# Performance work log

Measured on AMD Instinct MI355X. Metric: run time of the kernel, lower is better.

Reference implementation:

```python
import jax, jax.numpy as jnp
from jax import lax
import numpy as np

B, T = 16, 256
E, H, V = 512, 1024, 32000

def setup_inputs() -> dict:
    key = jax.random.key(0)
    ks = jax.random.split(key, 10)
    s = lambda fan_in: 1.0 / np.sqrt(fan_in)
    return {
        "z": jax.random.normal(ks[0], (B, H), dtype=jnp.float32),
        "x": jax.random.randint(ks[1], (B, T), 0, V, dtype=jnp.int64),
        "emb_table": jax.random.normal(ks[2], (V, E), dtype=jnp.float32) * 0.02,
        "W_init": jax.random.uniform(ks[3], (H, H), jnp.float32, -s(H), s(H)),
        "b_init": jnp.zeros((H,), jnp.float32),
        "W_ih": jax.random.uniform(ks[4], (3 * H, E), jnp.float32, -s(H), s(H)),
        "W_hh": jax.random.uniform(ks[5], (3 * H, H), jnp.float32, -s(H), s(H)),
        "b_ih": jax.random.uniform(ks[6], (3 * H,), jnp.float32, -s(H), s(H)),
        "b_hh": jax.random.uniform(ks[7], (3 * H,), jnp.float32, -s(H), s(H)),
        "W_out": jax.random.uniform(ks[8], (V, H), jnp.float32, -s(H), s(H)),
        "b_out": jnp.zeros((V,), jnp.float32),
    }

def reference(z, x, emb_table, W_init, b_init, W_ih, W_hh, b_ih, b_hh, W_out, b_out):
    # h0 = tanh(aff_init_lm(z))
    h0 = jnp.tanh(z @ W_init.T + b_init)  # [B, H]
    xe = emb_table[x]                      # [B, T, E] embedding lookup
    # Precompute input-side gate projections for all timesteps (no recurrence on input side)
    gi_all = jnp.einsum('bte,ge->btg', xe, W_ih) + b_ih  # [B, T, 3H]

    def step(h, gi):
        gh = h @ W_hh.T + b_hh                 # [B, 3H]
        ir, iz, inn = jnp.split(gi, 3, axis=-1)
        hr, hz, hn = jnp.split(gh, 3, axis=-1)
        r = jax.nn.sigmoid(ir + hr)
        zg = jax.nn.sigmoid(iz + hz)
        n = jnp.tanh(inn + r * hn)
        h_new = (1.0 - zg) * n + zg * h
        # Original module emits aff_out_x(h[j]) (state BEFORE consuming token j),
        # so we output the PREVIOUS hidden state at each step.
        return h_new, h

    _, hs_prev = lax.scan(step, h0, jnp.swapaxes(gi_all, 0, 1))  # [T, B, H] = h0..h_{T-1}
    hs = jnp.swapaxes(hs_prev, 0, 1)                              # [B, T, H]
    logits = jnp.einsum('bth,vh->btv', hs, W_out) + b_out         # [B, T, V]
    return logits
```

## Files before the change

kernel.cpp:

```cpp
#include <hip/hip_runtime.h>

typedef __attribute__((ext_vector_type(8))) short bf16x8;
typedef __attribute__((ext_vector_type(8))) unsigned short ushort8;
typedef __attribute__((ext_vector_type(4))) float f32x4;
typedef __attribute__((ext_vector_type(4))) int i32x4;

__device__ __forceinline__ unsigned short f2bf(float f) {
  union { float f; unsigned u; } v; v.f = f;
  unsigned r = (v.u + 0x7FFFu + ((v.u >> 16) & 1u)) >> 16;
  return (unsigned short)r;
}
__device__ __forceinline__ float bf2f(unsigned short h) {
  union { unsigned u; float f; } v; v.u = ((unsigned)h) << 16;
  return v.f;
}
__device__ __forceinline__ float sigm(float x) { return 1.f / (1.f + __expf(-x)); }
__device__ __forceinline__ float tanh_(float x) { return 1.f - 2.f / (__expf(2.f * x) + 1.f); }

__device__ __forceinline__ i32x4 ld_coh_b128(const void* p) {
  i32x4 r;
  asm volatile("global_load_dwordx4 %0, %1, off sc0 sc1" : "=v"(r) : "v"(p) : "memory");
  return r;
}
__device__ __forceinline__ unsigned ld_coh_u16(const void* p) {
  unsigned r;
  asm volatile("global_load_ushort %0, %1, off sc0 sc1" : "=v"(r) : "v"(p) : "memory");
  return r;
}
__device__ __forceinline__ void st_coh_b128(void* p, i32x4 v) {
  asm volatile("global_store_dwordx4 %0, %1, off sc0 sc1" :: "v"(p), "v"(v) : "memory");
}
__device__ __forceinline__ void st_coh_b16(void* p, unsigned v) {
  asm volatile("global_store_short %0, %1, off sc0 sc1" :: "v"(p), "v"(v) : "memory");
}
__device__ __forceinline__ void wait_vm0_fence() {
  asm volatile("s_waitcnt vmcnt(0)" ::: "memory");
  __builtin_amdgcn_sched_barrier(0);
}

#define GLDS(g, l) __builtin_amdgcn_global_load_lds( \
    (const __attribute__((address_space(1))) unsigned int*)(g), \
    (__attribute__((address_space(3))) unsigned int*)(l), 16, 0, 0)

__global__ __launch_bounds__(256) void prep(
    const int* __restrict__ x, const float* __restrict__ emb, unsigned short* __restrict__ xe,
    const float* __restrict__ z, const float* __restrict__ Wi, const float* __restrict__ bi,
    float* __restrict__ h0f, unsigned short* __restrict__ hb16,
    const float* __restrict__ Wih, unsigned short* __restrict__ WihB,
    const float* __restrict__ Wout, unsigned short* __restrict__ WoutB) {
  const int tid = threadIdx.x;
  const unsigned bid = blockIdx.x;
  if (bid < 2048) {
    const int r = (bid << 1) + (tid >> 7);
    const int b = r & 15, t = r >> 4;
    const int tok = x[b * 256 + t];
    const int c = tid & 127;
    const float4 v = ((const float4*)(emb + (size_t)tok * 512))[c];
    ushort4 o; o.x = f2bf(v.x); o.y = f2bf(v.y); o.z = f2bf(v.z); o.w = f2bf(v.w);
    ((ushort4*)(xe + (size_t)r * 512))[c] = o;
  } else if (bid < 2112) {
    const int idx = (bid - 2048) * 256 + tid;
    const int b = idx & 15, i = idx >> 4;
    const float4* wr = (const float4*)(Wi + (size_t)i * 1024);
    const float4* zr = (const float4*)(z + (size_t)b * 1024);
    float acc = bi[i];
#pragma unroll 4
    for (int k = 0; k < 256; ++k) {
      float4 w = wr[k], zv = zr[k];
      acc += w.x * zv.x + w.y * zv.y + w.z * zv.z + w.w * zv.w;
    }
    const float h = tanh_(acc);
    h0f[(size_t)b * 1024 + i] = h;
    hb16[((i >> 4) << 8) + (b << 4) + (i & 15)] = f2bf(h);
  } else if (bid < 3648) {
    const int i = (int)(bid - 2112) * 256 + tid;
    const float4 v = ((const float4*)Wih)[i];
    ushort4 o; o.x = f2bf(v.x); o.y = f2bf(v.y); o.z = f2bf(v.z); o.w = f2bf(v.w);
    ((ushort4*)WihB)[i] = o;
  } else {
    for (int i = (int)(bid - 3648) * 256 + tid; i < 32000 * 1024 / 4; i += 512 * 256) {
      const float4 v = ((const float4*)Wout)[i];
      ushort4 o; o.x = f2bf(v.x); o.y = f2bf(v.y); o.z = f2bf(v.z); o.w = f2bf(v.w);
      ((ushort4*)WoutB)[i] = o;
    }
  }
}

__global__ __launch_bounds__(512, 1) void mega(
    const float* __restrict__ Whh, const float* __restrict__ bhh,
    unsigned short* __restrict__ gi, const float* __restrict__ h0f,
    unsigned short* __restrict__ hb16, unsigned short* __restrict__ hs,
    unsigned int* __restrict__ flags, unsigned int* __restrict__ gicnt,
    const unsigned short* __restrict__ xe, const unsigned short* __restrict__ WihB,
    const float* __restrict__ bih,
    const unsigned short* __restrict__ WoutB, const float* __restrict__ bout,
    float* __restrict__ out) {
  __shared__ __align__(16) char lds[65536];
  const int tid = threadIdx.x, lane = tid & 63, wave = tid >> 6;

  if (blockIdx.x < 64) {
    const int j = blockIdx.x;
    if (tid >= 256) {
      for (int t = 0; t < 256; ++t) { __syncthreads(); if (t < 255) __syncthreads(); }
      __syncthreads();
      return;
    }
    float (*ghp)[16][48] = (float (*)[16][48])lds;
    unsigned short (*hsl)[16] = (unsigned short (*)[16])(lds + 12288);

    const int lr = lane & 15;
    const int hi8 = (lane >> 4) << 3;
    const int kw = wave << 8;

    bf16x8 wf[3][8];
#pragma unroll
    for (int n = 0; n < 3; ++n) {
      const float* wrow = Whh + (size_t)(n * 1024 + (j << 4) + lr) * 1024 + kw + hi8;
#pragma unroll
      for (int ki = 0; ki < 8; ++ki) {
        const float4 u = *(const float4*)(wrow + ki * 32);
        const float4 v = *(const float4*)(wrow + ki * 32 + 4);
        bf16x8 w;
        w[0] = (short)f2bf(u.x); w[1] = (short)f2bf(u.y);
        w[2] = (short)f2bf(u.z); w[3] = (short)f2bf(u.w);
        w[4] = (short)f2bf(v.x); w[5] = (short)f2bf(v.y);
        w[6] = (short)f2bf(v.z); w[7] = (short)f2bf(v.w);
        wf[n][ki] = w;
      }
    }

    const int b = tid >> 4, c = tid & 15;
    const int cg = (j << 4) + c;
    float hreg = h0f[(size_t)b * 1024 + cg];
    const float br = bhh[cg], bz = bhh[1024 + cg], bn = bhh[2048 + cg];

    for (int t = 0; t < 256; ++t) {
      {
        long guard = 0;
        for (;;) {
          bool ok = true;
          if (t > 0) {
            const unsigned f = __hip_atomic_load(&flags[lane << 5], __ATOMIC_RELAXED,
                                                 __HIP_MEMORY_SCOPE_AGENT);
            ok = (f >= (unsigned)t);
          }
          const unsigned g2 = __hip_atomic_load(&gicnt[(t >> 3) << 5], __ATOMIC_RELAXED,
                                                __HIP_MEMORY_SCOPE_AGENT);
          ok = ok && (g2 >= 24u);
          if (__all(ok)) break;
          __builtin_amdgcn_s_sleep(1);
          if (++guard > (1L << 20)) break;
        }
      }

      const unsigned short* base = hb16 + ((t & 1) << 14);
      i32x4 hv[8];
#pragma unroll
      for (int ki = 0; ki < 8; ++ki) {
        const int kk = kw + (ki << 5) + hi8;
        hv[ki] = ld_coh_b128(base + ((kk >> 4) << 8) + (lr << 4) + (kk & 15));
      }
      const char* gbase = (const char*)gi + ((size_t)((t << 4) + b) * 3072 + cg) * 2;
      const unsigned uir = ld_coh_u16(gbase);
      const unsigned uiz = ld_coh_u16(gbase + 2048);
      const unsigned uin = ld_coh_u16(gbase + 4096);
      wait_vm0_fence();

      f32x4 acc[3] = {};
#pragma unroll
      for (int ki = 0; ki < 8; ++ki) {
        const bf16x8 af = __builtin_bit_cast(bf16x8, hv[ki]);
#pragma unroll
        for (int n = 0; n < 3; ++n)
          acc[n] = __builtin_amdgcn_mfma_f32_16x16x32_bf16(af, wf[n][ki], acc[n], 0, 0, 0);
      }
#pragma unroll
      for (int n = 0; n < 3; ++n)
#pragma unroll
        for (int q = 0; q < 4; ++q)
          ghp[wave][(lane >> 4) * 4 + q][n * 16 + lr] = acc[n][q];
      __syncthreads();

      const float ir = bf2f((unsigned short)uir);
      const float iz = bf2f((unsigned short)uiz);
      const float inn = bf2f((unsigned short)uin);
      const float hr = ghp[0][b][c]      + ghp[1][b][c]      + ghp[2][b][c]      + ghp[3][b][c];
      const float hz = ghp[0][b][16 + c] + ghp[1][b][16 + c] + ghp[2][b][16 + c] + ghp[3][b][16 + c];
      const float hn = ghp[0][b][32 + c] + ghp[1][b][32 + c] + ghp[2][b][32 + c] + ghp[3][b][32 + c];
      const float rg = sigm(ir + hr + br);
      const float zg = sigm(iz + hz + bz);
      const float ng = tanh_(inn + rg * (hn + bn));
      const float hprev = hreg;
      hreg = (1.f - zg) * ng + zg * hprev;

      if (t < 255) {
        hsl[b][c] = f2bf(hreg);
        __syncthreads();
        unsigned short* nb = hb16 + (((t + 1) & 1) << 14) + (j << 8);
        if (tid < 32) {
          const i32x4 v = *(const i32x4*)&hsl[tid >> 1][(tid & 1) << 3];
          st_coh_b128(nb + (tid << 3), v);
        }
        if (wave == 0)
          asm volatile("s_waitcnt vmcnt(0)" ::: "memory");
        if (tid == 0)
          __hip_atomic_store(&flags[j << 5], (unsigned)(t + 1),
                             __ATOMIC_RELAXED, __HIP_MEMORY_SCOPE_AGENT);
      }

      st_coh_b16(hs + ((size_t)((t << 4) + b) << 10) + cg, (unsigned)f2bf(hprev));
    }
    asm volatile("s_waitcnt vmcnt(0)" ::: "memory");
    __syncthreads();
    if (tid == 0)
      __hip_atomic_store(&flags[j << 5], 1024u, __ATOMIC_RELAXED, __HIP_MEMORY_SCOPE_AGENT);
    return;
  }

  if (blockIdx.x < 832) {
    const int g = blockIdx.x - 64;
    const int tm = g / 24, tn = g % 24;
    const long row0 = (long)tm << 7, col0 = (long)tn << 7;
    char* As = lds;
    char* Bs = lds + 8192;
    char* Ct = lds + 16384;

    const int sr = tid >> 2, sk = (tid & 3) << 3;
    const unsigned short* Abase = xe + (row0 + sr) * 512 + sk;
    const unsigned short* Bbase = WihB + (col0 + sr) * 512 + sk;
    char* ldsA = As + wave * 1024;
    char* ldsB = Bs + wave * 1024;

    const int wm2 = (wave >> 2) << 6, wn2 = (wave & 3) << 5;
    const int lr = lane & 15, lk = (lane >> 4) << 3;
    f32x4 acc[4][2] = {};

    for (int k0 = 0; k0 < 512; k0 += 32) {
      __syncthreads();
      GLDS(Abase + k0, ldsA);
      GLDS(Bbase + k0, ldsB);
      __syncthreads();
      bf16x8 af[4], bfr[2];
#pragma unroll
      for (int i = 0; i < 4; ++i)
        af[i] = *(const bf16x8*)(As + ((wm2 + i * 16 + lr) * 32 + lk) * 2);
#pragma unroll
      for (int jj = 0; jj < 2; ++jj)
        bfr[jj] = *(const bf16x8*)(Bs + ((wn2 + jj * 16 + lr) * 32 + lk) * 2);
#pragma unroll
      for (int i = 0; i < 4; ++i)
#pragma unroll
        for (int jj = 0; jj < 2; ++jj)
          acc[i][jj] = __builtin_amdgcn_mfma_f32_16x16x32_bf16(af[i], bfr[jj], acc[i][jj], 0, 0, 0);
    }

    const int lq = (lane >> 4) << 2;
    float bias0 = bih[col0 + wn2 + lr], bias1 = bih[col0 + wn2 + 16 + lr];
    __syncthreads();
#pragma unroll
    for (int i = 0; i < 4; ++i)
#pragma unroll
      for (int jj = 0; jj < 2; ++jj)
#pragma unroll
        for (int q = 0; q < 4; ++q)
          *(unsigned short*)(Ct + (wm2 + i * 16 + lq + q) * 256
                                + ((wn2 + jj * 16 + lr) << 1)) =
              f2bf(acc[i][jj][q] + (jj ? bias1 : bias0));
    __syncthreads();
#pragma unroll
    for (int k2 = 0; k2 < 4; ++k2) {
      const int s2 = (k2 << 9) + tid;
      const int row = s2 >> 4, colb = (s2 & 15) << 4;
      st_coh_b128((char*)gi + (size_t)(row0 + row) * 6144 + (col0 << 1) + colb,
                  *(const i32x4*)(Ct + row * 256 + colb));
    }
    asm volatile("s_waitcnt vmcnt(0)" ::: "memory");
    __syncthreads();
    if (tid == 0)
      __hip_atomic_fetch_add(&gicnt[tm << 5], 1u, __ATOMIC_RELAXED,
                             __HIP_MEMORY_SCOPE_AGENT);
    return;
  }

  const int gb = blockIdx.x - 832;
  const int bm = gb / 125, bn = gb % 125;
  const long row0 = (long)bm << 8, col0 = (long)bn << 8;

  {
    unsigned thr = (unsigned)(16 * bm + 17); if (thr > 255u) thr = 1024u;
    if (wave == 0) {
      long guard = 0;
      for (;;) {
        const unsigned f = __hip_atomic_load(&flags[lane << 5], __ATOMIC_RELAXED,
                                             __HIP_MEMORY_SCOPE_AGENT);
        if (__all(f >= thr)) break;
        __builtin_amdgcn_s_sleep(32);
        if (++guard > (1L << 22)) break;
      }
    }
    __syncthreads();
  }

  const int wm = wave >> 2, wn = wave & 3;
  const int arow = tid >> 1, ahalf = (tid & 1) << 5;
  const char* Ab = (const char*)hs + ((row0 + arow) << 11) + ahalf;
  const int awz0 = ((arow << 6) + ahalf) ^ ((arow & 12) << 2);
  const int awz1 = ((arow << 6) + ahalf + 16) ^ ((arow & 12) << 2);
  const int srow = tid >> 2, skb = (tid & 3) << 4;
  auto stageB = [&](int sp, int rr) {
    const int row = (rr << 7) + srow;
    const int kbu = skb ^ ((row & 12) << 2);
    const char* g = (const char*)WoutB + ((col0 + row) << 11) + (sp << 6) + kbu;
    char* l = lds + ((sp & 1) << 15) + 16384 + (rr << 13) + (wave << 10);
    GLDS(g, l);
  };
  const int lr = lane & 15, ko = (lane >> 4) << 4;
  auto rdA = [&](int buf, int mrep) {
    const int rt = (wm << 7) + (mrep << 4) + lr;
    const int a = (rt << 6) + ko;
    return *(const bf16x8*)(lds + (buf << 15) + (a ^ ((rt & 12) << 2)));
  };
  auto rdB = [&](int buf, int nrep) {
    const int rt = (wn << 6) + (nrep << 4) + lr;
    const int a = (rt << 6) + ko;
    return *(const bf16x8*)(lds + (buf << 15) + 16384 + (a ^ ((rt & 12) << 2)));
  };

  f32x4 acc[8][4] = {};
  i32x4 rA0 = ld_coh_b128(Ab);
  i32x4 rA1 = ld_coh_b128(Ab + 16);
  stageB(0, 0); stageB(0, 1);

  for (int s = 0; s < 32; ++s) {
    const int buf = s & 1;
    if (s < 31) {
      stageB(s + 1, 0); stageB(s + 1, 1);
      asm volatile("s_waitcnt vmcnt(2)" ::: "memory");
    } else {
      asm volatile("s_waitcnt vmcnt(0)" ::: "memory");
    }
    __builtin_amdgcn_sched_barrier(0);
    *(i32x4*)(lds + (buf << 15) + awz0) = rA0;
    *(i32x4*)(lds + (buf << 15) + awz1) = rA1;
    if (s < 31) {
      rA0 = ld_coh_b128(Ab + ((s + 1) << 6));
      rA1 = ld_coh_b128(Ab + ((s + 1) << 6) + 16);
    }
    asm volatile("s_waitcnt lgkmcnt(0)" ::: "memory");
    __builtin_amdgcn_sched_barrier(0);
    __builtin_amdgcn_s_barrier();

    bf16x8 bfr[4], af[4], af2[4];
#pragma unroll
    for (int n = 0; n < 4; ++n) bfr[n] = rdB(buf, n);
#pragma unroll
    for (int m = 0; m < 4; ++m) af[m] = rdA(buf, m);
    asm volatile("s_waitcnt lgkmcnt(0)" ::: "memory");
    __builtin_amdgcn_sched_barrier(0);
    __builtin_amdgcn_s_setprio(1);
#pragma unroll
    for (int m = 0; m < 4; ++m)
#pragma unroll
      for (int n = 0; n < 4; ++n)
        acc[m][n] = __builtin_amdgcn_mfma_f32_16x16x32_bf16(af[m], bfr[n], acc[m][n], 0, 0, 0);
    __builtin_amdgcn_s_setprio(0);
#pragma unroll
    for (int m = 0; m < 4; ++m) af2[m] = rdA(buf, m + 4);
    asm volatile("s_waitcnt lgkmcnt(0)" ::: "memory");
    __builtin_amdgcn_sched_barrier(0);
    __builtin_amdgcn_s_barrier();
    __builtin_amdgcn_s_setprio(1);
#pragma unroll
    for (int m = 0; m < 4; ++m)
#pragma unroll
      for (int n = 0; n < 4; ++n)
        acc[m + 4][n] = __builtin_amdgcn_mfma_f32_16x16x32_bf16(af2[m], bfr[n], acc[m + 4][n], 0, 0, 0);
    __builtin_amdgcn_s_setprio(0);
  }

  const int lq = (lane >> 4) << 2;
#pragma unroll
  for (int mr = 0; mr < 8; ++mr) {
#pragma unroll
    for (int q = 0; q < 4; ++q) {
      const int ar = (int)row0 + (wm << 7) + (mr << 4) + lq + q;
      const int tt = ar >> 4, bb = ar & 15;
      float* crow = out + ((size_t)bb * 256 + tt) * 32000;
#pragma unroll
      for (int nr = 0; nr < 4; ++nr) {
        const long cc = col0 + (wn << 6) + (nr << 4) + lr;
        crow[cc] = acc[mr][nr][q] + bout[cc];
      }
    }
  }
}

extern "C" void kernel_launch(void* const* d_in, const int* in_sizes, int n_in,
                              void* d_out, int out_size, void* d_ws, size_t ws_size,
                              hipStream_t stream) {
  const float* z     = (const float*)d_in[0];
  const int*   x     = (const int*)d_in[1];
  const float* emb   = (const float*)d_in[2];
  const float* Winit = (const float*)d_in[3];
  const float* binit = (const float*)d_in[4];
  const float* Wih   = (const float*)d_in[5];
  const float* Whh   = (const float*)d_in[6];
  const float* bih   = (const float*)d_in[7];
  const float* bhh   = (const float*)d_in[8];
  const float* Wout  = (const float*)d_in[9];
  const float* bout  = (const float*)d_in[10];
  float* out = (float*)d_out;

  char* ws = (char*)d_ws;
  size_t off = 0;
  auto alloc = [&](size_t bytes) { void* p = ws + off; off += (bytes + 255) & ~(size_t)255; return p; };
  unsigned int*   flags = (unsigned int*)alloc(64 * 128);
  unsigned int*   gicnt = (unsigned int*)alloc(32 * 128);
  unsigned short* xe    = (unsigned short*)alloc((size_t)4096 * 512 * 2);
  unsigned short* WihB  = (unsigned short*)alloc((size_t)3072 * 512 * 2);
  unsigned short* WoutB = (unsigned short*)alloc((size_t)32000 * 1024 * 2);
  unsigned short* giB   = (unsigned short*)alloc((size_t)4096 * 3072 * 2);
  unsigned short* hsB   = (unsigned short*)alloc((size_t)4096 * 1024 * 2);
  float*          h0f   = (float*)alloc((size_t)16 * 1024 * 4);
  unsigned short* hb16  = (unsigned short*)alloc((size_t)2 * 16 * 1024 * 2);
  (void)ws_size; (void)in_sizes; (void)n_in; (void)out_size;

  hipMemsetAsync(flags, 0, 64 * 128 + 32 * 128, stream);

  prep<<<dim3(4160), 256, 0, stream>>>(x, emb, xe, z, Winit, binit, h0f, hb16,
                                       Wih, WihB, Wout, WoutB);

  mega<<<dim3(2832), 512, 0, stream>>>(Whh, bhh, giB, h0f, hb16, hsB, flags, gicnt,
                                       xe, WihB, bih, WoutB, bout, out);
}
```

Measured before the change: 1.012 ms.

## Convert mega kernel to persistent workers with atomic work queue

Replaces the 2832-block grid with 256 blocks where non-recurrence blocks loop, fetching tile indices from a global atomic counter (gi GEMM tiles first, then output GEMM tiles). This guarantees the input-projection tiles are processed before output tiles, keeps blocks resident, and avoids block launch and scheduling overhead. It adds an atomic per tile and an extra barrier, and workers may stall while spinning on recurrence flags.

```diff
diff --git a/kernel.cpp b/kernel.cpp
--- a/kernel.cpp
+++ b/kernel.cpp
@@ -91,6 +91,7 @@
     unsigned short* __restrict__ gi, const float* __restrict__ h0f,
     unsigned short* __restrict__ hb16, unsigned short* __restrict__ hs,
     unsigned int* __restrict__ flags, unsigned int* __restrict__ gicnt,
+    unsigned int* __restrict__ qhead,
     const unsigned short* __restrict__ xe, const unsigned short* __restrict__ WihB,
     const float* __restrict__ bih,
     const unsigned short* __restrict__ WoutB, const float* __restrict__ bout,
@@ -217,181 +218,191 @@
     return;
   }
 
-  if (blockIdx.x < 832) {
-    const int g = blockIdx.x - 64;
-    const int tm = g / 24, tn = g % 24;
-    const long row0 = (long)tm << 7, col0 = (long)tn << 7;
-    char* As = lds;
-    char* Bs = lds + 8192;
-    char* Ct = lds + 16384;
-
-    const int sr = tid >> 2, sk = (tid & 3) << 3;
-    const unsigned short* Abase = xe + (row0 + sr) * 512 + sk;
-    const unsigned short* Bbase = WihB + (col0 + sr) * 512 + sk;
-    char* ldsA = As + wave * 1024;
-    char* ldsB = Bs + wave * 1024;
-
-    const int wm2 = (wave >> 2) << 6, wn2 = (wave & 3) << 5;
-    const int lr = lane & 15, lk = (lane >> 4) << 3;
-    f32x4 acc[4][2] = {};
-
-    for (int k0 = 0; k0 < 512; k0 += 32) {
-      __syncthreads();
-      GLDS(Abase + k0, ldsA);
-      GLDS(Bbase + k0, ldsB);
-      __syncthreads();
-      bf16x8 af[4], bfr[2];
-#pragma unroll
-      for (int i = 0; i < 4; ++i)
-        af[i] = *(const bf16x8*)(As + ((wm2 + i * 16 + lr) * 32 + lk) * 2);
-#pragma unroll
-      for (int jj = 0; jj < 2; ++jj)
-        bfr[jj] = *(const bf16x8*)(Bs + ((wn2 + jj * 16 + lr) * 32 + lk) * 2);
-#pragma unroll
-      for (int i = 0; i < 4; ++i)
-#pragma unroll
-        for (int jj = 0; jj < 2; ++jj)
-          acc[i][jj] = __builtin_amdgcn_mfma_f32_16x16x32_bf16(af[i], bfr[jj], acc[i][jj], 0, 0, 0);
-    }
-
-    const int lq = (lane >> 4) << 2;
-    float bias0 = bih[col0 + wn2 + lr], bias1 = bih[col0 + wn2 + 16 + lr];
-    __syncthreads();
-#pragma unroll
-    for (int i = 0; i < 4; ++i)
-#pragma unroll
-      for (int jj = 0; jj < 2; ++jj)
-#pragma unroll
-        for (int q = 0; q < 4; ++q)
-          *(unsigned short*)(Ct + (wm2 + i * 16 + lq + q) * 256
-                                + ((wn2 + jj * 16 + lr) << 1)) =
-              f2bf(acc[i][jj][q] + (jj ? bias1 : bias0));
-    __syncthreads();
-#pragma unroll
-    for (int k2 = 0; k2 < 4; ++k2) {
-      const int s2 = (k2 << 9) + tid;
-      const int row = s2 >> 4, colb = (s2 & 15) << 4;
-      st_coh_b128((char*)gi + (size_t)(row0 + row) * 6144 + (col0 << 1) + colb,
-                  *(const i32x4*)(Ct + row * 256 + colb));
-    }
-    asm volatile("s_waitcnt vmcnt(0)" ::: "memory");
-    __syncthreads();
-    if (tid == 0)
-      __hip_atomic_fetch_add(&gicnt[tm << 5], 1u, __ATOMIC_RELAXED,
-                             __HIP_MEMORY_SCOPE_AGENT);
-    return;
-  }
-
-  const int gb = blockIdx.x - 832;
-  const int bm = gb / 125, bn = gb % 125;
-  const long row0 = (long)bm << 8, col0 = (long)bn << 8;
-
-  {
-    unsigned thr = (unsigned)(16 * bm + 17); if (thr > 255u) thr = 1024u;
-    if (wave == 0) {
-      long guard = 0;
-      for (;;) {
-        const unsigned f = __hip_atomic_load(&flags[lane << 5], __ATOMIC_RELAXED,
-                                             __HIP_MEMORY_SCOPE_AGENT);
-        if (__all(f >= thr)) break;
-        __builtin_amdgcn_s_sleep(32);
-        if (++guard > (1L << 22)) break;
-      }
-    }
-    __syncthreads();
-  }
-
+  __shared__ unsigned qk_sh;
   const int wm = wave >> 2, wn = wave & 3;
+  const int lr = lane & 15, ko = (lane >> 4) << 4;
   const int arow = tid >> 1, ahalf = (tid & 1) << 5;
-  const char* Ab = (const char*)hs + ((row0 + arow) << 11) + ahalf;
   const int awz0 = ((arow << 6) + ahalf) ^ ((arow & 12) << 2);
   const int awz1 = ((arow << 6) + ahalf + 16) ^ ((arow & 12) << 2);
   const int srow = tid >> 2, skb = (tid & 3) << 4;
-  auto stageB = [&](int sp, int rr) {
-    const int row = (rr << 7) + srow;
-    const int kbu = skb ^ ((row & 12) << 2);
-    const char* g = (const char*)WoutB + ((col0 + row) << 11) + (sp << 6) + kbu;
-    char* l = lds + ((sp & 1) << 15) + 16384 + (rr << 13) + (wave << 10);
-    GLDS(g, l);
-  };
-  const int lr = lane & 15, ko = (lane >> 4) << 4;
-  auto rdA = [&](int buf, int mrep) {
-    const int rt = (wm << 7) + (mrep << 4) + lr;
-    const int a = (rt << 6) + ko;
-    return *(const bf16x8*)(lds + (buf << 15) + (a ^ ((rt & 12) << 2)));
-  };
-  auto rdB = [&](int buf, int nrep) {
-    const int rt = (wn << 6) + (nrep << 4) + lr;
-    const int a = (rt << 6) + ko;
-    return *(const bf16x8*)(lds + (buf << 15) + 16384 + (a ^ ((rt & 12) << 2)));
-  };
-
-  f32x4 acc[8][4] = {};
-  i32x4 rA0 = ld_coh_b128(Ab);
-  i32x4 rA1 = ld_coh_b128(Ab + 16);
-  stageB(0, 0); stageB(0, 1);
-
-  for (int s = 0; s < 32; ++s) {
-    const int buf = s & 1;
-    if (s < 31) {
-      stageB(s + 1, 0); stageB(s + 1, 1);
-      asm volatile("s_waitcnt vmcnt(2)" ::: "memory");
-    } else {
+  const int lq = (lane >> 4) << 2;
+
+  for (;;) {
+    if (tid == 0)
+      qk_sh = __hip_atomic_fetch_add(qhead, 1u, __ATOMIC_RELAXED, __HIP_MEMORY_SCOPE_AGENT);
+    __syncthreads();
+    const unsigned k = qk_sh;
+    if (k >= 2768u) return;
+
+    if (k < 768u) {
+      const int tm = (int)(k / 24), tn = (int)(k % 24);
+      const long row0 = (long)tm << 7, col0 = (long)tn << 7;
+      char* As = lds;
+      char* Bs = lds + 8192;
+      char* Ct = lds + 16384;
+
+      const int sr = tid >> 2, sk = (tid & 3) << 3;
+      const unsigned short* Abase = xe + (row0 + sr) * 512 + sk;
+      const unsigned short* Bbase = WihB + (col0 + sr) * 512 + sk;
+      char* ldsA = As + wave * 1024;
+      char* ldsB = Bs + wave * 1024;
+
+      const int wm2 = (wave >> 2) << 6, wn2 = (wave & 3) << 5;
+      const int lk = (lane >> 4) << 3;
+      f32x4 acc[4][2] = {};
+
+      for (int k0 = 0; k0 < 512; k0 += 32) {
+        __syncthreads();
+        GLDS(Abase + k0, ldsA);
+        GLDS(Bbase + k0, ldsB);
+        __syncthreads();
+        bf16x8 af[4], bfr[2];
+#pragma unroll
+        for (int i = 0; i < 4; ++i)
+          af[i] = *(const bf16x8*)(As + ((wm2 + i * 16 + lr) * 32 + lk) * 2);
+#pragma unroll
+        for (int jj = 0; jj < 2; ++jj)
+          bfr[jj] = *(const bf16x8*)(Bs + ((wn2 + jj * 16 + lr) * 32 + lk) * 2);
+#pragma unroll
+        for (int i = 0; i < 4; ++i)
+#pragma unroll
+          for (int jj = 0; jj < 2; ++jj)
+            acc[i][jj] = __builtin_amdgcn_mfma_f32_16x16x32_bf16(af[i], bfr[jj], acc[i][jj], 0, 0, 0);
+      }
+
+      const float bias0 = bih[col0 + wn2 + lr], bias1 = bih[col0 + wn2 + 16 + lr];
+      __syncthreads();
+#pragma unroll
+      for (int i = 0; i < 4; ++i)
+#pragma unroll
+        for (int jj = 0; jj < 2; ++jj)
+#pragma unroll
+          for (int q = 0; q < 4; ++q)
+            *(unsigned short*)(Ct + (wm2 + i * 16 + lq + q) * 256
+                                  + ((wn2 + jj * 16 + lr) << 1)) =
+                f2bf(acc[i][jj][q] + (jj ? bias1 : bias0));
+      __syncthreads();
+#pragma unroll
+      for (int k2 = 0; k2 < 4; ++k2) {
+        const int s2 = (k2 << 9) + tid;
+        const int row = s2 >> 4, colb = (s2 & 15) << 4;
+        st_coh_b128((char*)gi + (size_t)(row0 + row) * 6144 + (col0 << 1) + colb,
+                    *(const i32x4*)(Ct + row * 256 + colb));
+      }
       asm volatile("s_waitcnt vmcnt(0)" ::: "memory");
-    }
-    __builtin_amdgcn_sched_barrier(0);
-    *(i32x4*)(lds + (buf << 15) + awz0) = rA0;
-    *(i32x4*)(lds + (buf << 15) + awz1) = rA1;
-    if (s < 31) {
-      rA0 = ld_coh_b128(Ab + ((s + 1) << 6));
-      rA1 = ld_coh_b128(Ab + ((s + 1) << 6) + 16);
-    }
-    asm volatile("s_waitcnt lgkmcnt(0)" ::: "memory");
-    __builtin_amdgcn_sched_barrier(0);
-    __builtin_amdgcn_s_barrier();
-
-    bf16x8 bfr[4], af[4], af2[4];
-#pragma unroll
-    for (int n = 0; n < 4; ++n) bfr[n] = rdB(buf, n);
-#pragma unroll
-    for (int m = 0; m < 4; ++m) af[m] = rdA(buf, m);
-    asm volatile("s_waitcnt lgkmcnt(0)" ::: "memory");
-    __builtin_amdgcn_sched_barrier(0);
-    __builtin_amdgcn_s_setprio(1);
-#pragma unroll
-    for (int m = 0; m < 4; ++m)
-#pragma unroll
-      for (int n = 0; n < 4; ++n)
-        acc[m][n] = __builtin_amdgcn_mfma_f32_16x16x32_bf16(af[m], bfr[n], acc[m][n], 0, 0, 0);
-    __builtin_amdgcn_s_setprio(0);
-#pragma unroll
-    for (int m = 0; m < 4; ++m) af2[m] = rdA(buf, m + 4);
-    asm volatile("s_waitcnt lgkmcnt(0)" ::: "memory");
-    __builtin_amdgcn_sched_barrier(0);
-    __builtin_amdgcn_s_barrier();
-    __builtin_amdgcn_s_setprio(1);
-#pragma unroll
-    for (int m = 0; m < 4; ++m)
-#pragma unroll
-      for (int n = 0; n < 4; ++n)
-        acc[m + 4][n] = __builtin_amdgcn_mfma_f32_16x16x32_bf16(af2[m], bfr[n], acc[m + 4][n], 0, 0, 0);
-    __builtin_amdgcn_s_setprio(0);
-  }
-
-  const int lq = (lane >> 4) << 2;
-#pragma unroll
-  for (int mr = 0; mr < 8; ++mr) {
-#pragma unroll
-    for (int q = 0; q < 4; ++q) {
-      const int ar = (int)row0 + (wm << 7) + (mr << 4) + lq + q;
-      const int tt = ar >> 4, bb = ar & 15;
-      float* crow = out + ((size_t)bb * 256 + tt) * 32000;
-#pragma unroll
-      for (int nr = 0; nr < 4; ++nr) {
-        const long cc = col0 + (wn << 6) + (nr << 4) + lr;
-        crow[cc] = acc[mr][nr][q] + bout[cc];
-      }
-    }
+      __syncthreads();
+      if (tid == 0)
+        __hip_atomic_fetch_add(&gicnt[tm << 5], 1u, __ATOMIC_RELAXED,
+                               __HIP_MEMORY_SCOPE_AGENT);
+      __syncthreads();
+      continue;
+    }
+
+    const unsigned lk2 = k - 768u;
+    const int bm = (int)(lk2 / 125), bn = (int)(lk2 % 125);
+    const long row0 = (long)bm << 8, col0 = (long)bn << 8;
+
+    {
+      unsigned thr = (unsigned)(16 * bm + 17); if (thr > 255u) thr = 1024u;
+      if (wave == 0) {
+        long guard = 0;
+        for (;;) {
+          const unsigned f = __hip_atomic_load(&flags[lane << 5], __ATOMIC_RELAXED,
+                                               __HIP_MEMORY_SCOPE_AGENT);
+          if (__all(f >= thr)) break;
+          __builtin_amdgcn_s_sleep(32);
+          if (++guard > (1L << 22)) break;
+        }
+      }
+      __syncthreads();
+    }
+
+    const char* Ab = (const char*)hs + ((row0 + arow) << 11) + ahalf;
+    auto stageB = [&](int sp, int rr) {
+      const int row = (rr << 7) + srow;
+      const int kbu = skb ^ ((row & 12) << 2);
+      const char* g = (const char*)WoutB + ((col0 + row) << 11) + (sp << 6) + kbu;
+      char* l = lds + ((sp & 1) << 15) + 16384 + (rr << 13) + (wave << 10);
+      GLDS(g, l);
+    };
+    auto rdA = [&](int buf, int mrep) {
+      const int rt = (wm << 7) + (mrep << 4) + lr;
+      const int a = (rt << 6) + ko;
+      return *(const bf16x8*)(lds + (buf << 15) + (a ^ ((rt & 12) << 2)));
+    };
+    auto rdB = [&](int buf, int nrep) {
+      const int rt = (wn << 6) + (nrep << 4) + lr;
+      const int a = (rt << 6) + ko;
+      return *(const bf16x8*)(lds + (buf << 15) + 16384 + (a ^ ((rt & 12) << 2)));
+    };
+
+    f32x4 acc[8][4] = {};
+    i32x4 rA0 = ld_coh_b128(Ab);
+    i32x4 rA1 = ld_coh_b128(Ab + 16);
+    stageB(0, 0); stageB(0, 1);
+
+    for (int s = 0; s < 32; ++s) {
+      const int buf = s & 1;
+      if (s < 31) {
+        stageB(s + 1, 0); stageB(s + 1, 1);
+        asm volatile("s_waitcnt vmcnt(2)" ::: "memory");
+      } else {
+        asm volatile("s_waitcnt vmcnt(0)" ::: "memory");
+      }
+      __builtin_amdgcn_sched_barrier(0);
+      *(i32x4*)(lds + (buf << 15) + awz0) = rA0;
+      *(i32x4*)(lds + (buf << 15) + awz1) = rA1;
+      if (s < 31) {
+        rA0 = ld_coh_b128(Ab + ((s + 1) << 6));
+        rA1 = ld_coh_b128(Ab + ((s + 1) << 6) + 16);
+      }
+      asm volatile("s_waitcnt lgkmcnt(0)" ::: "memory");
+      __builtin_amdgcn_sched_barrier(0);
+      __builtin_amdgcn_s_barrier();
+
+      bf16x8 bfr[4], af[4], af2[4];
+#pragma unroll
+      for (int n = 0; n < 4; ++n) bfr[n] = rdB(buf, n);
+#pragma unroll
+      for (int m = 0; m < 4; ++m) af[m] = rdA(buf, m);
+      asm volatile("s_waitcnt lgkmcnt(0)" ::: "memory");
+      __builtin_amdgcn_sched_barrier(0);
+      __builtin_amdgcn_s_setprio(1);
+#pragma unroll
+      for (int m = 0; m < 4; ++m)
+#pragma unroll
+        for (int n = 0; n < 4; ++n)
+          acc[m][n] = __builtin_amdgcn_mfma_f32_16x16x32_bf16(af[m], bfr[n], acc[m][n], 0, 0, 0);
+      __builtin_amdgcn_s_setprio(0);
+#pragma unroll
+      for (int m = 0; m < 4; ++m) af2[m] = rdA(buf, m + 4);
+      asm volatile("s_waitcnt lgkmcnt(0)" ::: "memory");
+      __builtin_amdgcn_sched_barrier(0);
+      __builtin_amdgcn_s_barrier();
+      __builtin_amdgcn_s_setprio(1);
+#pragma unroll
+      for (int m = 0; m < 4; ++m)
+#pragma unroll
+        for (int n = 0; n < 4; ++n)
+          acc[m + 4][n] = __builtin_amdgcn_mfma_f32_16x16x32_bf16(af2[m], bfr[n], acc[m + 4][n], 0, 0, 0);
+      __builtin_amdgcn_s_setprio(0);
+    }
+
+#pragma unroll
+    for (int mr = 0; mr < 8; ++mr) {
+#pragma unroll
+      for (int q = 0; q < 4; ++q) {
+        const int ar = (int)row0 + (wm << 7) + (mr << 4) + lq + q;
+        const int tt = ar >> 4, bb = ar & 15;
+        float* crow = out + ((size_t)bb * 256 + tt) * 32000;
+#pragma unroll
+        for (int nr = 0; nr < 4; ++nr) {
+          const long cc = col0 + (wn << 6) + (nr << 4) + lr;
+          crow[cc] = acc[mr][nr][q] + bout[cc];
+        }
+      }
+    }
+    __syncthreads();
   }
 }
 
@@ -416,6 +427,7 @@
   auto alloc = [&](size_t bytes) { void* p = ws + off; off += (bytes + 255) & ~(size_t)255; return p; };
   unsigned int*   flags = (unsigned int*)alloc(64 * 128);
   unsigned int*   gicnt = (unsigned int*)alloc(32 * 128);
+  unsigned int*   qhead = (unsigned int*)alloc(256);
   unsigned short* xe    = (unsigned short*)alloc((size_t)4096 * 512 * 2);
   unsigned short* WihB  = (unsigned short*)alloc((size_t)3072 * 512 * 2);
   unsigned short* WoutB = (unsigned short*)alloc((size_t)32000 * 1024 * 2);
@@ -425,11 +437,11 @@
   unsigned short* hb16  = (unsigned short*)alloc((size_t)2 * 16 * 1024 * 2);
   (void)ws_size; (void)in_sizes; (void)n_in; (void)out_size;
 
-  hipMemsetAsync(flags, 0, 64 * 128 + 32 * 128, stream);
+  hipMemsetAsync(flags, 0, 64 * 128 + 32 * 128 + 256, stream);
 
   prep<<<dim3(4160), 256, 0, stream>>>(x, emb, xe, z, Winit, binit, h0f, hb16,
                                        Wih, WihB, Wout, WoutB);
 
-  mega<<<dim3(2832), 512, 0, stream>>>(Whh, bhh, giB, h0f, hb16, hsB, flags, gicnt,
-                                       xe, WihB, bih, WoutB, bout, out);
-}
+  mega<<<dim3(256), 512, 0, stream>>>(Whh, bhh, giB, h0f, hb16, hsB, flags, gicnt,
+                                      qhead, xe, WihB, bih, WoutB, bout, out);
+}
```

Measured after the change: 1.024 ms. Within noise of the previous version (+1.1%).
